# Performance work log

Hardware: AMD Instinct MI355X
Metric: run time of the kernel (lower is better)

## Reference

```python
import jax, jax.numpy as jnp
import numpy as np

KERNEL_SIZE = 37  # int((6*20-7)//3) = 37, already odd
PAD = (KERNEL_SIZE - 1) // 2  # 18


def moving_avg(x):
    """Edge-replicated moving average along token axis. x: [B, T, C]."""
    front = jnp.repeat(x[:, :1, :], PAD, axis=1)
    end = jnp.repeat(x[:, -1:, :], PAD, axis=1)
    xp = jnp.concatenate([front, x, end], axis=1)  # [B, T+2*PAD, C]
    cs = jnp.cumsum(xp, axis=1)
    cs = jnp.concatenate([jnp.zeros_like(cs[:, :1, :]), cs], axis=1)
    # window sums: length (T+2*PAD+1) - KERNEL_SIZE = T
    return (cs[:, KERNEL_SIZE:, :] - cs[:, :-KERNEL_SIZE, :]) / KERNEL_SIZE


def setup_inputs() -> dict:
    key = jax.random.key(0)
    ks = jax.random.split(key, 5)
    B, T, Cin, Cout = 4096, 17, 512, 512
    scale = 1.0 / np.sqrt(Cin)
    x = jax.random.normal(ks[0], (B, T, Cin), dtype=jnp.float32)
    W_seasonal = jax.random.uniform(ks[1], (T, Cout, Cin), jnp.float32, -scale, scale)
    b_seasonal = jax.random.uniform(ks[2], (T, Cout), jnp.float32, -scale, scale)
    W_trend = jax.random.uniform(ks[3], (T, Cout, Cin), jnp.float32, -scale, scale)
    b_trend = jax.random.uniform(ks[4], (T, Cout), jnp.float32, -scale, scale)
    return {"x": x, "W_seasonal": W_seasonal, "b_seasonal": b_seasonal,
            "W_trend": W_trend, "b_trend": b_trend}


def reference(x, W_seasonal, b_seasonal, W_trend, b_trend):
    trend = moving_avg(x)            # [B, T, Cin]
    seasonal = x - trend             # [B, T, Cin]
    # per-token (grouped) linear layers as one batched einsum
    s_out = jnp.einsum('btc,tdc->btd', seasonal, W_seasonal) + b_seasonal[None]
    t_out = jnp.einsum('btc,tdc->btd', trend, W_trend) + b_trend[None]
    return s_out + t_out
```

## Files before the change

### kernel.cpp

```cpp
#include <hip/hip_runtime.h>
#include <stdint.h>

#define B_N 4096
#define T_N 17
#define C_N 512
#define KTOT 1024

typedef __bf16 bf16x8 __attribute__((ext_vector_type(8)));
typedef float  f32x4  __attribute__((ext_vector_type(4)));

__device__ __forceinline__ unsigned short f2b(float f){
  unsigned u = __float_as_uint(f);
  return (unsigned short)((u + 0x7fffu + ((u >> 16) & 1u)) >> 16);
}
__device__ __forceinline__ unsigned pk2(float a, float b){
  return (unsigned)f2b(a) | ((unsigned)f2b(b) << 16);
}

__device__ __forceinline__ void gll16(const void* g, void* l){
  __builtin_amdgcn_global_load_lds(
      (const __attribute__((address_space(1))) unsigned int*)g,
      (__attribute__((address_space(3))) unsigned int*)l, 16, 0, 0);
}

#define BAR()   __builtin_amdgcn_s_barrier()
#define VMC(n)  do{ asm volatile("s_waitcnt vmcnt(" #n ")" ::: "memory"); \
                    __builtin_amdgcn_sched_barrier(0); }while(0)
#define FENCE() asm volatile("" ::: "memory")

__global__ __launch_bounds__(256) void prep_w(
    const float* __restrict__ Ws, const float* __restrict__ Wt,
    unsigned short* __restrict__ wcat)
{
  const size_t i8 = ((size_t)blockIdx.x * 256 + threadIdx.x) * 8;
  const int t   = (int)(i8 >> 18);
  const int rem = (int)(i8 & 262143);
  const int d   = rem >> 9;
  const int c   = rem & 511;
  float4 a0 = *(const float4*)(Ws + i8);
  float4 a1 = *(const float4*)(Ws + i8 + 4);
  float4 b0 = *(const float4*)(Wt + i8);
  float4 b1 = *(const float4*)(Wt + i8 + 4);
  uint4 oa, od;
  oa.x = pk2(a0.x, a0.y); oa.y = pk2(a0.z, a0.w);
  oa.z = pk2(a1.x, a1.y); oa.w = pk2(a1.z, a1.w);
  od.x = pk2(b0.x - a0.x, b0.y - a0.y); od.y = pk2(b0.z - a0.z, b0.w - a0.w);
  od.z = pk2(b1.x - a1.x, b1.y - a1.y); od.w = pk2(b1.z - a1.z, b1.w - a1.w);
  unsigned short* base = wcat + ((size_t)(t * C_N + d)) * KTOT + c;
  *(uint4*)base = oa;
  *(uint4*)(base + C_N) = od;
}

__global__ __launch_bounds__(256) void prep_a(
    const float* __restrict__ x, unsigned short* __restrict__ acat)
{
  const int idx = blockIdx.x * 256 + threadIdx.x;
  const int b = idx >> 6;
  const int c = (idx & 63) << 3;
  const float* xp = x + (size_t)b * (T_N * C_N) + c;
  float s[8] = {0,0,0,0,0,0,0,0};
  float f0[8], fl[8];
#pragma unroll
  for (int tt = 0; tt < T_N; ++tt){
    float4 w0 = *(const float4*)(xp + (size_t)tt * C_N);
    float4 w1 = *(const float4*)(xp + (size_t)tt * C_N + 4);
    float f[8] = {w0.x, w0.y, w0.z, w0.w, w1.x, w1.y, w1.z, w1.w};
    uint4 o;
    o.x = pk2(f[0],f[1]); o.y = pk2(f[2],f[3]);
    o.z = pk2(f[4],f[5]); o.w = pk2(f[6],f[7]);
    *(uint4*)(acat + ((size_t)tt * B_N + b) * KTOT + c) = o;
    if (tt == 0){
#pragma unroll
      for (int i=0;i<8;++i) f0[i] = f[i];
    }
    if (tt == T_N-1){
#pragma unroll
      for (int i=0;i<8;++i) fl[i] = f[i];
    }
#pragma unroll
    for (int i=0;i<8;++i) s[i] += f[i];
  }
  const float inv = 1.0f / 37.0f;
  float uu[8], vv[8];
#pragma unroll
  for (int i=0;i<8;++i){
    uu[i] = (s[i] + 18.0f * f0[i] + 2.0f * fl[i]) * inv;
    vv[i] = (fl[i] - f0[i]) * inv;
  }
#pragma unroll
  for (int tt = 0; tt < T_N; ++tt){
    const float tfv = (float)tt;
    float tr[8];
#pragma unroll
    for (int i=0;i<8;++i) tr[i] = fmaf(tfv, vv[i], uu[i]);
    uint4 o;
    o.x = pk2(tr[0],tr[1]); o.y = pk2(tr[2],tr[3]);
    o.z = pk2(tr[4],tr[5]); o.w = pk2(tr[6],tr[7]);
    *(uint4*)(acat + ((size_t)tt * B_N + b) * KTOT + C_N + c) = o;
  }
}

__global__ __launch_bounds__(256, 2) void gemm4(
    const unsigned short* __restrict__ acat,
    const unsigned short* __restrict__ wcat,
    const float* __restrict__ bs,
    const float* __restrict__ bt,
    float* __restrict__ out)
{
  __shared__ alignas(16) unsigned short A_lds[2][128][64];
  __shared__ alignas(16) unsigned short B_lds[2][128][64];

  const int tid = threadIdx.x;
  const int bid = blockIdx.x;
  const int wg = (bid & 7) * 272 + (bid >> 3);
  const int t  = wg >> 7;
  const int rm = wg & 127;
  const int mt = rm >> 2;
  const int nt = rm & 3;
  const int m0 = mt << 7;
  const int n0 = nt << 7;

  const int lane = tid & 63;
  const int wave = tid >> 6;
  const int wr = wave >> 1;
  const int wc = wave & 1;
  const int lr = lane & 15;
  const int g  = lane >> 4;

  const int row0 = tid >> 3;
  const int cc0  = tid & 7;
  const int cswz = ((cc0 ^ (row0 & 7)) << 3);
  const unsigned short* gA0 = acat + ((size_t)t * B_N + m0 + row0) * KTOT + cswz;
  const unsigned short* gB0 = wcat + ((size_t)t * C_N + n0 + row0) * KTOT + cswz;
  unsigned short* lA0 = &A_lds[0][0][0] + tid * 8;
  unsigned short* lB0 = &B_lds[0][0][0] + tid * 8;

  auto stage = [&](int bb, int kt){
#pragma unroll
    for (int r = 0; r < 4; ++r)
      gll16(gB0 + (size_t)kt * 64 + r * 32768, lB0 + bb * 8192 + r * 2048);
#pragma unroll
    for (int r = 0; r < 4; ++r)
      gll16(gA0 + (size_t)kt * 64 + r * 32768, lA0 + bb * 8192 + r * 2048);
  };

  const int sw  = lr & 7;
  const int ca0 = (( g    ) ^ sw) << 3;
  const int ca1 = ((4 | g ) ^ sw) << 3;
  const unsigned short* Arow = &A_lds[0][wr * 64 + lr][0];
  const unsigned short* Brow = &B_lds[0][wc * 64 + lr][0];

  f32x4 acc[4][4];
#pragma unroll
  for (int i=0;i<4;++i)
#pragma unroll
    for (int j=0;j<4;++j){ f32x4 z = {0.f,0.f,0.f,0.f}; acc[i][j] = z; }

  stage(0, 0);
  stage(1, 1);
  VMC(8);
  BAR();

#pragma unroll 1
  for (int it = 0; it < 16; ++it){
    const int bb = it & 1;
    bf16x8 af[4][2], bf[4][2];
#pragma unroll
    for (int i=0;i<4;++i){
      const unsigned short* pB = Brow + bb * 8192 + i * 1024;
      bf[i][0] = *(const bf16x8*)(pB + ca0);
      bf[i][1] = *(const bf16x8*)(pB + ca1);
    }
#pragma unroll
    for (int i=0;i<4;++i){
      const unsigned short* pA = Arow + bb * 8192 + i * 1024;
      af[i][0] = *(const bf16x8*)(pA + ca0);
      af[i][1] = *(const bf16x8*)(pA + ca1);
    }

    __builtin_amdgcn_s_setprio(1);
#pragma unroll
    for (int mi=0;mi<4;++mi)
#pragma unroll
      for (int ni=0;ni<4;++ni){
        acc[mi][ni] = __builtin_amdgcn_mfma_f32_16x16x32_bf16(af[mi][0], bf[ni][0], acc[mi][ni],0,0,0);
        acc[mi][ni] = __builtin_amdgcn_mfma_f32_16x16x32_bf16(af[mi][1], bf[ni][1], acc[mi][ni],0,0,0);
      }
    __builtin_amdgcn_s_setprio(0);

    FENCE();
    BAR();
    if (it < 14){
      stage(bb, it + 2);
      VMC(8);
    } else if (it == 14){
      VMC(0);
    }
    BAR();
  }

  float bias[4];
#pragma unroll
  for (int ni=0;ni<4;++ni){
    const size_t bi = (size_t)t * C_N + n0 + wc*64 + ni*16 + lr;
    bias[ni] = bs[bi] + bt[bi];
  }

#pragma unroll
  for (int mi=0;mi<4;++mi){
#pragma unroll
    for (int rr=0;rr<4;++rr){
      const int m = m0 + wr*64 + mi*16 + g*4 + rr;
      float* op = out + ((size_t)m * T_N + t) * C_N + n0 + wc*64 + lr;
#pragma unroll
      for (int ni=0;ni<4;++ni)
        op[ni*16] = acc[mi][ni][rr] + bias[ni];
    }
  }
}

extern "C" void kernel_launch(void* const* d_in, const int* in_sizes, int n_in,
                              void* d_out, int out_size, void* d_ws, size_t ws_size,
                              hipStream_t stream)
{
  const float* x   = (const float*)d_in[0];
  const float* Wsl = (const float*)d_in[1];
  const float* bsl = (const float*)d_in[2];
  const float* Wtr = (const float*)d_in[3];
  const float* btr = (const float*)d_in[4];
  float* out = (float*)d_out;

  const size_t WCAT_BYTES = (size_t)T_N * C_N * KTOT * 2;
  char* ws = (char*)d_ws;
  unsigned short* wcat = (unsigned short*)ws;
  unsigned short* acat = (unsigned short*)(ws + WCAT_BYTES);

  prep_w <<<dim3(2176), dim3(256), 0, stream>>>(Wsl, Wtr, wcat);
  prep_a <<<dim3(1024), dim3(256), 0, stream>>>(x, acat);
  gemm4  <<<dim3(2176), dim3(256), 0, stream>>>(acat, wcat, bsl, btr, out);
  (void)in_sizes; (void)n_in; (void)out_size; (void)ws_size;
}
```

Before: 413.4 us.

## Enlarge GEMM tile to 256x256 with 8 waves and interleaved ping-pong load/MFMA schedule

Replaces the 128x128 four-wave GEMM with a 256x256 tile run by 8 waves (2x4), each wave computing 128x64. The K loop is split into quarter-tile MFMA clusters. Global-to-LDS staging for the next K slices is interleaved between clusters, with barriers and lgkmcnt waits so loads overlap compute. This raises data reuse per LDS byte and hides memory latency. In exchange it uses more accumulator registers, adds many barriers, and launches fewer workgroups (544), which may hurt occupancy and load balance.

```diff
diff --git a/kernel.cpp b/kernel.cpp
--- a/kernel.cpp
+++ b/kernel.cpp
@@ -24,9 +24,10 @@
 }
 
 #define BAR()   __builtin_amdgcn_s_barrier()
+#define LGKM0() do{ asm volatile("s_waitcnt lgkmcnt(0)" ::: "memory"); \
+                    __builtin_amdgcn_sched_barrier(0); }while(0)
 #define VMC(n)  do{ asm volatile("s_waitcnt vmcnt(" #n ")" ::: "memory"); \
                     __builtin_amdgcn_sched_barrier(0); }while(0)
-#define FENCE() asm volatile("" ::: "memory")
 
 __global__ __launch_bounds__(256) void prep_w(
     const float* __restrict__ Ws, const float* __restrict__ Wt,
@@ -100,30 +101,29 @@
   }
 }
 
-__global__ __launch_bounds__(256, 2) void gemm4(
+__global__ __launch_bounds__(512, 2) void gemm8p(
     const unsigned short* __restrict__ acat,
     const unsigned short* __restrict__ wcat,
     const float* __restrict__ bs,
     const float* __restrict__ bt,
     float* __restrict__ out)
 {
-  __shared__ alignas(16) unsigned short A_lds[2][128][64];
-  __shared__ alignas(16) unsigned short B_lds[2][128][64];
+  __shared__ alignas(16) unsigned short A_lds[2][256][64];
+  __shared__ alignas(16) unsigned short B_lds[2][256][64];
 
   const int tid = threadIdx.x;
   const int bid = blockIdx.x;
-  const int wg = (bid & 7) * 272 + (bid >> 3);
-  const int t  = wg >> 7;
-  const int rm = wg & 127;
-  const int mt = rm >> 2;
-  const int nt = rm & 3;
-  const int m0 = mt << 7;
-  const int n0 = nt << 7;
+  const int wg = (bid & 7) * 68 + (bid >> 3);
+  const int t  = wg >> 5;
+  const int mt = (wg >> 1) & 15;
+  const int nt = wg & 1;
+  const int m0 = mt << 8;
+  const int n0 = nt << 8;
 
   const int lane = tid & 63;
   const int wave = tid >> 6;
-  const int wr = wave >> 1;
-  const int wc = wave & 1;
+  const int wr = wave >> 2;
+  const int wc = wave & 3;
   const int lr = lane & 15;
   const int g  = lane >> 4;
 
@@ -135,67 +135,116 @@
   unsigned short* lA0 = &A_lds[0][0][0] + tid * 8;
   unsigned short* lB0 = &B_lds[0][0][0] + tid * 8;
 
-  auto stage = [&](int bb, int kt){
-#pragma unroll
-    for (int r = 0; r < 4; ++r)
-      gll16(gB0 + (size_t)kt * 64 + r * 32768, lB0 + bb * 8192 + r * 2048);
-#pragma unroll
-    for (int r = 0; r < 4; ++r)
-      gll16(gA0 + (size_t)kt * 64 + r * 32768, lA0 + bb * 8192 + r * 2048);
+  auto stA2 = [&](int bb, int kt, int mh){
+    gll16(gA0 + (size_t)kt * 64 + (size_t)(mh * 64) * KTOT,
+          lA0 + bb * 16384 + mh * 4096);
+    gll16(gA0 + (size_t)kt * 64 + (size_t)(mh * 64 + 128) * KTOT,
+          lA0 + bb * 16384 + (mh + 2) * 4096);
+  };
+  auto stB2 = [&](int bb, int kt, int hf){
+    gll16(gB0 + (size_t)kt * 64 + (size_t)(hf * 128) * KTOT,
+          lB0 + bb * 16384 + hf * 8192);
+    gll16(gB0 + (size_t)kt * 64 + (size_t)(hf * 128 + 64) * KTOT,
+          lB0 + bb * 16384 + hf * 8192 + 4096);
   };
 
   const int sw  = lr & 7;
   const int ca0 = (( g    ) ^ sw) << 3;
   const int ca1 = ((4 | g ) ^ sw) << 3;
-  const unsigned short* Arow = &A_lds[0][wr * 64 + lr][0];
-  const unsigned short* Brow = &B_lds[0][wc * 64 + lr][0];
-
-  f32x4 acc[4][4];
-#pragma unroll
-  for (int i=0;i<4;++i)
+  const unsigned short* Arow = &A_lds[0][wr * 128 + lr][0];
+  const unsigned short* Brow = &B_lds[0][wc * 64  + lr][0];
+
+  bf16x8 aF[4][2], bF0[2][2], bF1[2][2];
+  f32x4 acc[8][4];
+#pragma unroll
+  for (int i=0;i<8;++i)
 #pragma unroll
     for (int j=0;j<4;++j){ f32x4 z = {0.f,0.f,0.f,0.f}; acc[i][j] = z; }
 
-  stage(0, 0);
-  stage(1, 1);
+  auto rdA = [&](int bb, int mh){
+#pragma unroll
+    for (int mi=0;mi<4;++mi){
+      const unsigned short* p = Arow + bb * 16384 + mh * 4096 + mi * 1024;
+      aF[mi][0] = *(const bf16x8*)(p + ca0);
+      aF[mi][1] = *(const bf16x8*)(p + ca1);
+    }
+  };
+  auto rdB = [&](int bb, int nh, bf16x8 (&dst)[2][2]){
+#pragma unroll
+    for (int ni=0;ni<2;++ni){
+      const unsigned short* p = Brow + bb * 16384 + nh * 2048 + ni * 1024;
+      dst[ni][0] = *(const bf16x8*)(p + ca0);
+      dst[ni][1] = *(const bf16x8*)(p + ca1);
+    }
+  };
+  auto cluster = [&](int mh, int nh, bf16x8 (&bF)[2][2]){
+    __builtin_amdgcn_s_setprio(1);
+#pragma unroll
+    for (int mi=0;mi<4;++mi)
+#pragma unroll
+      for (int ni=0;ni<2;++ni){
+        f32x4* a = &acc[mh*4+mi][nh*2+ni];
+        *a = __builtin_amdgcn_mfma_f32_16x16x32_bf16(aF[mi][0], bF[ni][0], *a,0,0,0);
+        *a = __builtin_amdgcn_mfma_f32_16x16x32_bf16(aF[mi][1], bF[ni][1], *a,0,0,0);
+      }
+    __builtin_amdgcn_s_setprio(0);
+  };
+
+  stA2(0, 0, 0); stA2(0, 0, 1); stB2(0, 0, 0); stB2(0, 0, 1);
+  stA2(1, 1, 0); stA2(1, 1, 1); stB2(1, 1, 0); stB2(1, 1, 1);
   VMC(8);
   BAR();
 
 #pragma unroll 1
-  for (int it = 0; it < 16; ++it){
-    const int bb = it & 1;
-    bf16x8 af[4][2], bf[4][2];
-#pragma unroll
-    for (int i=0;i<4;++i){
-      const unsigned short* pB = Brow + bb * 8192 + i * 1024;
-      bf[i][0] = *(const bf16x8*)(pB + ca0);
-      bf[i][1] = *(const bf16x8*)(pB + ca1);
-    }
-#pragma unroll
-    for (int i=0;i<4;++i){
-      const unsigned short* pA = Arow + bb * 8192 + i * 1024;
-      af[i][0] = *(const bf16x8*)(pA + ca0);
-      af[i][1] = *(const bf16x8*)(pA + ca1);
-    }
-
-    __builtin_amdgcn_s_setprio(1);
-#pragma unroll
-    for (int mi=0;mi<4;++mi)
-#pragma unroll
-      for (int ni=0;ni<4;++ni){
-        acc[mi][ni] = __builtin_amdgcn_mfma_f32_16x16x32_bf16(af[mi][0], bf[ni][0], acc[mi][ni],0,0,0);
-        acc[mi][ni] = __builtin_amdgcn_mfma_f32_16x16x32_bf16(af[mi][1], bf[ni][1], acc[mi][ni],0,0,0);
-      }
-    __builtin_amdgcn_s_setprio(0);
-
-    FENCE();
-    BAR();
-    if (it < 14){
-      stage(bb, it + 2);
-      VMC(8);
-    } else if (it == 14){
-      VMC(0);
-    }
+  for (int i = 0; i < 8; ++i){
+    const int s1 = 2*i+1, s2 = 2*i+2, s3 = 2*i+3;
+    const bool st1 = (s1 >= 2), st2 = (s2 <= 15), st3 = (s3 <= 15);
+
+    rdA(0, 0); rdB(0, 0, bF0);
+    if (st1){ stB2(1, s1, 0); stA2(1, s1, 1); }
+    BAR(); LGKM0();
+    cluster(0, 0, bF0);
+    BAR();
+
+    rdB(0, 1, bF1);
+    if (st1){ stB2(1, s1, 1); }
+    BAR(); LGKM0();
+    cluster(0, 1, bF1);
+    BAR();
+
+    rdA(0, 1);
+    if (st2){ stA2(0, s2, 0); }
+    BAR(); LGKM0();
+    cluster(1, 0, bF0);
+    BAR();
+
+    BAR(); LGKM0();
+    cluster(1, 1, bF1);
+    if (i < 7) { VMC(2); } else { VMC(0); }
+    BAR();
+
+    rdA(1, 0); rdB(1, 0, bF0);
+    if (st2){ stA2(0, s2, 1); }
+    BAR(); LGKM0();
+    cluster(0, 0, bF0);
+    BAR();
+
+    rdB(1, 1, bF1);
+    if (st2){ stB2(0, s2, 0); }
+    BAR(); LGKM0();
+    cluster(0, 1, bF1);
+    BAR();
+
+    rdA(1, 1);
+    if (st2){ stB2(0, s2, 1); }
+    BAR(); LGKM0();
+    cluster(1, 0, bF0);
+    BAR();
+
+    if (st3){ stA2(1, s3, 0); }
+    BAR(); LGKM0();
+    cluster(1, 1, bF1);
+    if (i < 7) { VMC(2); } else { VMC(0); }
     BAR();
   }
 
@@ -207,10 +256,10 @@
   }
 
 #pragma unroll
-  for (int mi=0;mi<4;++mi){
+  for (int mi=0;mi<8;++mi){
 #pragma unroll
     for (int rr=0;rr<4;++rr){
-      const int m = m0 + wr*64 + mi*16 + g*4 + rr;
+      const int m = m0 + wr*128 + mi*16 + g*4 + rr;
       float* op = out + ((size_t)m * T_N + t) * C_N + n0 + wc*64 + lr;
 #pragma unroll
       for (int ni=0;ni<4;++ni)
@@ -237,6 +286,6 @@
 
   prep_w <<<dim3(2176), dim3(256), 0, stream>>>(Wsl, Wtr, wcat);
   prep_a <<<dim3(1024), dim3(256), 0, stream>>>(x, acat);
-  gemm4  <<<dim3(2176), dim3(256), 0, stream>>>(acat, wcat, bsl, btr, out);
+  gemm8p <<<dim3(544),  dim3(512), 0, stream>>>(acat, wcat, bsl, btr, out);
   (void)in_sizes; (void)n_in; (void)out_size; (void)ws_size;
 }
```

Result: faster. 405.3 us (-2.0%).
